# Performance work log

Hardware: AMD Instinct MI355X
Metric: run time of the kernel (lower is better)

Reference implementation:

```python
import jax, jax.numpy as jnp
import numpy as np

K = 3
STRIDE = 1
PAD = 1
EPS = 1e-5


def conv2d(x, w, b):
    # x [B,C,H,W], w [O,I,K,K], b [O]
    y = jax.lax.conv_general_dilated(
        x, w, (STRIDE, STRIDE), [(PAD, PAD), (PAD, PAD)],
        dimension_numbers=("NCHW", "OIHW", "NCHW"))
    return y + b[None, :, None, None]


def _bilinear_sample(img, py, px):
    # img [C,H,W]; py,px [KK,Ho,Wo] continuous coords; zero outside bounds
    H, W = img.shape[1], img.shape[2]
    y0 = jnp.floor(py)
    x0 = jnp.floor(px)
    wy1 = py - y0
    wx1 = px - x0
    wy0 = 1.0 - wy1
    wx0 = 1.0 - wx1

    def gather(yi, xi):
        valid = (yi >= 0) & (yi < H) & (xi >= 0) & (xi < W)
        yc = jnp.clip(yi, 0, H - 1).astype(jnp.int32)
        xc = jnp.clip(xi, 0, W - 1).astype(jnp.int32)
        v = img[:, yc, xc]  # [C,KK,Ho,Wo]
        return v * valid.astype(img.dtype)[None]

    out = (gather(y0, x0) * (wy0 * wx0)[None]
           + gather(y0, x0 + 1) * (wy0 * wx1)[None]
           + gather(y0 + 1, x0) * (wy1 * wx0)[None]
           + gather(y0 + 1, x0 + 1) * (wy1 * wx1)[None])
    return out  # [C,KK,Ho,Wo]


def deform_conv_bn_act(x, w_off, b_off, w_mod, b_mod, w_dc, gamma, beta):
    B, C, H, W = x.shape
    Cout = w_dc.shape[0]
    KK = K * K
    Ho = (H + 2 * PAD - K) // STRIDE + 1
    Wo = (W + 2 * PAD - K) // STRIDE + 1

    offset = conv2d(x, w_off, b_off)                 # [B,2*KK,Ho,Wo]
    modulation = jax.nn.sigmoid(conv2d(x, w_mod, b_mod))  # [B,KK,Ho,Wo]

    off = offset.reshape(B, KK, 2, Ho, Wo)
    dy, dx = off[:, :, 0], off[:, :, 1]              # [B,KK,Ho,Wo]

    ky = jnp.repeat(jnp.arange(K), K).astype(x.dtype)   # kernel row index per tap
    kx = jnp.tile(jnp.arange(K), K).astype(x.dtype)     # kernel col index per tap
    base_y = (jnp.arange(Ho, dtype=x.dtype) * STRIDE - PAD)[None, :, None] + ky[:, None, None]
    base_x = (jnp.arange(Wo, dtype=x.dtype) * STRIDE - PAD)[None, None, :] + kx[:, None, None]
    py = dy + base_y[None]                           # [B,KK,Ho,Wo]
    px = dx + base_x[None]

    sampled = jax.vmap(_bilinear_sample)(x, py, px)  # [B,C,KK,Ho,Wo]
    sampled = sampled * modulation[:, None]          # modulation per tap

    out = jnp.einsum("bckhw,ock->bohw", sampled, w_dc.reshape(Cout, C, KK))

    # BatchNorm (training-mode batch statistics, biased variance)
    mean = jnp.mean(out, axis=(0, 2, 3), keepdims=True)
    var = jnp.mean((out - mean) ** 2, axis=(0, 2, 3), keepdims=True)
    out = (out - mean) * jax.lax.rsqrt(var + EPS)
    out = out * gamma[None, :, None, None] + beta[None, :, None, None]

    return jax.nn.silu(out)


def setup_inputs() -> dict:
    key = jax.random.key(0)
    ks = jax.random.split(key, 8)
    B, Cin, Cout, H, W = 8, 128, 256, 64, 64
    x = jax.random.normal(ks[0], (B, Cin, H, W), dtype=jnp.float32)
    # small random offset/modulation weights (the literal init is all-zero, which
    # would make the deform conv degenerate to a plain conv)
    w_off = jax.random.normal(ks[1], (2 * K * K, Cin, K, K), dtype=jnp.float32) * 0.01
    b_off = jnp.zeros((2 * K * K,), dtype=jnp.float32)
    w_mod = jax.random.normal(ks[2], (K * K, Cin, K, K), dtype=jnp.float32) * 0.01
    b_mod = jnp.ones((K * K,), dtype=jnp.float32)
    fan_in = Cin * K * K
    w_dc = jax.random.normal(ks[3], (Cout, Cin, K, K), dtype=jnp.float32) / np.sqrt(fan_in)
    gamma = 1.0 + 0.1 * jax.random.normal(ks[4], (Cout,), dtype=jnp.float32)
    beta = 0.1 * jax.random.normal(ks[5], (Cout,), dtype=jnp.float32)
    return {"x": x, "w_off": w_off, "b_off": b_off, "w_mod": w_mod,
            "b_mod": b_mod, "w_dc": w_dc, "gamma": gamma, "beta": beta}


def reference(x, w_off, b_off, w_mod, b_mod, w_dc, gamma, beta):
    return deform_conv_bn_act(x, w_off, b_off, w_mod, b_mod, w_dc, gamma, beta)
```

## Files before the change

### kernel.cpp

```cpp
#include <hip/hip_runtime.h>
#include <hip/hip_bf16.h>
#include <math.h>

#define H_ 64
#define W_ 64
#define CIN 128
#define COUT 256
#define NB 8
#define KK9 9
#define NPIX 4096
#define KTOT 1152
#define NCK 36
#define KPAD 40

typedef short short8_t __attribute__((ext_vector_type(8)));
typedef float floatx4 __attribute__((ext_vector_type(4)));

__device__ __forceinline__ unsigned short f2bf(float f) {
    union { float f; unsigned u; } v; v.f = f;
    unsigned r = v.u + 0x7FFF + ((v.u >> 16) & 1);
    return (unsigned short)(r >> 16);
}
__device__ __forceinline__ float bf2f(unsigned short h) {
    union { unsigned u; float f; } v; v.u = ((unsigned)h) << 16;
    return v.f;
}

#if defined(__has_builtin)
#if __has_builtin(__builtin_amdgcn_global_load_lds)
#define HAVE_GLOAD_LDS 1
#endif
#endif

#ifdef HAVE_GLOAD_LDS
__device__ __forceinline__ void gload_lds16(const unsigned int* g, unsigned int* l) {
    __builtin_amdgcn_global_load_lds(
        (const __attribute__((address_space(1))) unsigned int*)g,
        (__attribute__((address_space(3))) unsigned int*)l, 16, 0, 0);
}
#endif

__global__ __launch_bounds__(256) void k_offmod(
    const float* __restrict__ x, const float* __restrict__ w_off,
    const float* __restrict__ b_off, const float* __restrict__ w_mod,
    const float* __restrict__ b_mod, float* __restrict__ ppy,
    float* __restrict__ ppx, float* __restrict__ pmod)
{
    __shared__ float xp[16][10][12];
    __shared__ float wb[27][16][12];
    const int t = threadIdx.x;
    const int tx = blockIdx.x, ty = blockIdx.y, b = blockIdx.z;
    const int q = t & 15, g = t >> 4;
    const int lpy = q >> 1, lpx4 = (q & 1) * 4;
    float acc[2][4] = {};

    for (int cc = 0; cc < CIN; cc += 16) {
        __syncthreads();
        for (int idx = t; idx < 1600; idx += 256) {
            int c = idx / 100, r = (idx % 100) / 10, col = idx % 10;
            int gy = ty * 8 - 1 + r, gx = tx * 8 - 1 + col;
            float v = 0.f;
            if (gy >= 0 && gy < H_ && gx >= 0 && gx < W_)
                v = x[((b * CIN + cc + c) * H_ + gy) * W_ + gx];
            xp[c][r][col] = v;
        }
        for (int idx = t; idx < 27 * 16 * 9; idx += 256) {
            int ch = idx / 144, rr = idx % 144, c = rr / 9, tap = rr % 9;
            wb[ch][c][tap] = (ch < 18)
                ? w_off[(ch * CIN + cc + c) * 9 + tap]
                : w_mod[((ch - 18) * CIN + cc + c) * 9 + tap];
        }
        __syncthreads();

        for (int c = 0; c < 16; ++c) {
            float xv[3][8];
            #pragma unroll
            for (int ky = 0; ky < 3; ++ky) {
                float4 v0 = *(const float4*)&xp[c][lpy + ky][lpx4];
                float4 v1 = *(const float4*)&xp[c][lpy + ky][lpx4 + 4];
                xv[ky][0] = v0.x; xv[ky][1] = v0.y; xv[ky][2] = v0.z; xv[ky][3] = v0.w;
                xv[ky][4] = v1.x; xv[ky][5] = v1.y; xv[ky][6] = v1.z; xv[ky][7] = v1.w;
            }
            #pragma unroll
            for (int i = 0; i < 2; ++i) {
                int ch = g + 16 * i;
                if (ch < 27) {
                    const float* wr = &wb[ch][c][0];
                    #pragma unroll
                    for (int ky = 0; ky < 3; ++ky)
                        #pragma unroll
                        for (int kx = 0; kx < 3; ++kx) {
                            float wv = wr[ky * 3 + kx];
                            #pragma unroll
                            for (int p = 0; p < 4; ++p)
                                acc[i][p] += xv[ky][p + kx] * wv;
                        }
                }
            }
        }
    }

    const int ho = ty * 8 + lpy;
    #pragma unroll
    for (int i = 0; i < 2; ++i) {
        int ch = g + 16 * i;
        if (ch >= 27) continue;
        #pragma unroll
        for (int p = 0; p < 4; ++p) {
            int wo = tx * 8 + lpx4 + p;
            int pix = ho * W_ + wo;
            if (ch < 18) {
                float v = acc[i][p] + b_off[ch];
                int kk = ch >> 1;
                if ((ch & 1) == 0)
                    ppy[(b * KK9 + kk) * NPIX + pix] = v + (float)(ho - 1 + kk / 3);
                else
                    ppx[(b * KK9 + kk) * NPIX + pix] = v + (float)(wo - 1 + kk % 3);
            } else {
                int km = ch - 18;
                float v = acc[i][p] + b_mod[km];
                pmod[(b * KK9 + km) * NPIX + pix] = 1.f / (1.f + expf(-v));
            }
        }
    }
}

__global__ __launch_bounds__(256) void k_prep(
    const float* __restrict__ w_dc, unsigned short* __restrict__ wsplit)
{
    int idx = blockIdx.x * 256 + threadIdx.x;
    int kl = idx % KPAD;
    int rest = idx / KPAD;
    int o = rest & 255;
    int rest2 = rest >> 8;
    int hl = rest2 & 1, ck = rest2 >> 1;
    unsigned short v = 0;
    if (kl < 32) {
        int kp = ck * 32 + kl;
        int kk = kp >> 7, c = kp & 127;
        float w = w_dc[o * KTOT + c * 9 + kk];
        unsigned short hi = f2bf(w);
        v = hl ? f2bf(w - bf2f(hi)) : hi;
    }
    wsplit[idx] = v;
}

__global__ __launch_bounds__(256, 2) void k_main(
    const float* __restrict__ x, const unsigned short* __restrict__ wsplit,
    const float* __restrict__ ppy, const float* __restrict__ ppx,
    const float* __restrict__ pmod, float* __restrict__ out,
    float* __restrict__ gsum, float* __restrict__ gsq)
{
    __shared__ __align__(16) unsigned short Wsp[2 * COUT * KPAD];
    __shared__ __align__(16) unsigned short Ssp[2 * 64 * KPAD];
    __shared__ float ppl[3][KK9][64];
    __shared__ float redS[COUT], redQ[COUT];

    const int t = threadIdx.x;
    const int b = blockIdx.x & 7;
    const int pix0 = (blockIdx.x >> 3) * 64;
    const int lane = t & 63, wm = t >> 6;

    for (int idx = t; idx < 3 * KK9 * 64; idx += 256) {
        int arr = idx / (KK9 * 64), rem = idx - arr * (KK9 * 64);
        int kk = rem >> 6, p = rem & 63;
        const float* src = (arr == 0) ? ppy : (arr == 1) ? ppx : pmod;
        ppl[arr][kk][p] = src[(b * KK9 + kk) * NPIX + pix0 + p];
    }
    __syncthreads();

    floatx4 acc[4][4] = {};
    const float* xb = x + b * CIN * NPIX;
    const int pxl = t & 63, kg = t >> 6;
    const int o_lane = lane & 15, g4 = lane >> 4;

    for (int kk = 0; kk < KK9; ++kk) {
        float py = ppl[0][kk][pxl];
        float px = ppl[1][kk][pxl];
        float m  = ppl[2][kk][pxl];
        float y0f = floorf(py), x0f = floorf(px);
        float wy1 = py - y0f, wx1 = px - x0f;
        float wy0 = 1.f - wy1, wx0 = 1.f - wx1;
        int y0 = (int)y0f, x0 = (int)x0f;
        bool y0v = (unsigned)y0 < (unsigned)H_;
        bool y1v = (unsigned)(y0 + 1) < (unsigned)H_;
        bool x0v = (unsigned)x0 < (unsigned)W_;
        bool x1v = (unsigned)(x0 + 1) < (unsigned)W_;
        float w00 = (y0v && x0v) ? wy0 * wx0 * m : 0.f;
        float w01 = (y0v && x1v) ? wy0 * wx1 * m : 0.f;
        float w10 = (y1v && x0v) ? wy1 * wx0 * m : 0.f;
        float w11 = (y1v && x1v) ? wy1 * wx1 * m : 0.f;
        int y0c = min(max(y0, 0), H_ - 1), y1c = min(max(y0 + 1, 0), H_ - 1);
        int x0c = min(max(x0, 0), W_ - 1), x1c = min(max(x0 + 1, 0), W_ - 1);
        int a00 = y0c * W_ + x0c, a01 = y0c * W_ + x1c;
        int a10 = y1c * W_ + x0c, a11 = y1c * W_ + x1c;

        for (int sub = 0; sub < 4; ++sub) {
            const int ck = kk * 4 + sub;
            __syncthreads();
            {
                const unsigned short* wsrc = wsplit + ck * (2 * COUT * KPAD);
#ifdef HAVE_GLOAD_LDS
                #pragma unroll
                for (int i = 0; i < 10; ++i) {
                    int slice = i * 4 + wm;
                    gload_lds16((const unsigned int*)(wsrc + slice * 512 + lane * 8),
                                (unsigned int*)(Wsp + slice * 512));
                }
#else
                const float4* s4 = (const float4*)wsrc;
                float4* d4 = (float4*)Wsp;
                #pragma unroll
                for (int i = 0; i < 10; ++i)
                    d4[i * 256 + t] = s4[i * 256 + t];
#endif
            }
            {
                const int c0 = sub * 32 + kg * 8;
                const float* pl = xb + c0 * NPIX;
                unsigned short hs[8], ls[8];
                #pragma unroll
                for (int j = 0; j < 8; ++j) {
                    float s = pl[a00] * w00 + pl[a01] * w01 +
                              pl[a10] * w10 + pl[a11] * w11;
                    union { float f; unsigned u; } su; su.f = s;
                    hs[j] = (unsigned short)(su.u >> 16);
                    union { unsigned u; float f; } hf; hf.u = su.u & 0xFFFF0000u;
                    union { float f; unsigned u; } du; du.f = s - hf.f;
                    ls[j] = (unsigned short)(du.u >> 16);
                    pl += NPIX;
                }
                union { unsigned short u[8]; short8_t v; } ph, plo;
                #pragma unroll
                for (int j = 0; j < 8; ++j) { ph.u[j] = hs[j]; plo.u[j] = ls[j]; }
                *(short8_t*)(Ssp + pxl * KPAD + kg * 8) = ph.v;
                *(short8_t*)(Ssp + 64 * KPAD + pxl * KPAD + kg * 8) = plo.v;
            }
            __syncthreads();

            short8_t bh[4], bl[4];
            #pragma unroll
            for (int ni = 0; ni < 4; ++ni) {
                int pxf = ni * 16 + o_lane;
                bh[ni] = *(const short8_t*)(Ssp + pxf * KPAD + g4 * 8);
                bl[ni] = *(const short8_t*)(Ssp + 64 * KPAD + pxf * KPAD + g4 * 8);
            }
            #pragma unroll
            for (int mi = 0; mi < 4; ++mi) {
                int of = wm * 64 + mi * 16 + o_lane;
                short8_t ah = *(const short8_t*)(Wsp + of * KPAD + g4 * 8);
                short8_t al = *(const short8_t*)(Wsp + COUT * KPAD + of * KPAD + g4 * 8);
                #pragma unroll
                for (int ni = 0; ni < 4; ++ni) {
                    acc[mi][ni] = __builtin_amdgcn_mfma_f32_16x16x32_bf16(
                        ah, bh[ni], acc[mi][ni], 0, 0, 0);
                    acc[mi][ni] = __builtin_amdgcn_mfma_f32_16x16x32_bf16(
                        ah, bl[ni], acc[mi][ni], 0, 0, 0);
                    acc[mi][ni] = __builtin_amdgcn_mfma_f32_16x16x32_bf16(
                        al, bh[ni], acc[mi][ni], 0, 0, 0);
                }
            }
        }
    }

    #pragma unroll
    for (int mi = 0; mi < 4; ++mi) {
        #pragma unroll
        for (int r = 0; r < 4; ++r) {
            float s = 0.f, q = 0.f;
            #pragma unroll
            for (int ni = 0; ni < 4; ++ni) {
                float v = acc[mi][ni][r];
                s += v; q += v * v;
            }
            s += __shfl_xor(s, 1); q += __shfl_xor(q, 1);
            s += __shfl_xor(s, 2); q += __shfl_xor(q, 2);
            s += __shfl_xor(s, 4); q += __shfl_xor(q, 4);
            s += __shfl_xor(s, 8); q += __shfl_xor(q, 8);
            if (o_lane == 0) {
                int o = wm * 64 + mi * 16 + g4 * 4 + r;
                redS[o] = s;
                redQ[o] = q;
            }
        }
    }
    __syncthreads();
    if (t < COUT) {
        atomicAdd(&gsum[t], redS[t]);
        atomicAdd(&gsq[t],  redQ[t]);
    }

    #pragma unroll
    for (int mi = 0; mi < 4; ++mi) {
        int o_base = wm * 64 + mi * 16 + g4 * 4;
        #pragma unroll
        for (int ni = 0; ni < 4; ++ni) {
            int px = pix0 + ni * 16 + o_lane;
            #pragma unroll
            for (int r = 0; r < 4; ++r)
                out[(b * COUT + o_base + r) * NPIX + px] = acc[mi][ni][r];
        }
    }
}

__global__ __launch_bounds__(256) void k_bnact(
    float* __restrict__ out, const float* __restrict__ gsum,
    const float* __restrict__ gsq, const float* __restrict__ gamma,
    const float* __restrict__ beta)
{
    int idx = blockIdx.x * 256 + threadIdx.x;
    int o = (idx >> 10) & 255;
    const float invn = 1.f / 32768.f;
    float mean = gsum[o] * invn;
    float var = gsq[o] * invn - mean * mean;
    float scale = gamma[o] * rsqrtf(var + 1e-5f);
    float shift = beta[o] - mean * scale;
    float4* p = (float4*)out;
    float4 v = p[idx];
    float y;
    y = v.x * scale + shift; v.x = y / (1.f + expf(-y));
    y = v.y * scale + shift; v.y = y / (1.f + expf(-y));
    y = v.z * scale + shift; v.z = y / (1.f + expf(-y));
    y = v.w * scale + shift; v.w = y / (1.f + expf(-y));
    p[idx] = v;
}

extern "C" void kernel_launch(void* const* d_in, const int* in_sizes, int n_in,
                              void* d_out, int out_size, void* d_ws, size_t ws_size,
                              hipStream_t stream)
{
    (void)in_sizes; (void)n_in; (void)out_size; (void)ws_size;
    const float* x     = (const float*)d_in[0];
    const float* w_off = (const float*)d_in[1];
    const float* b_off = (const float*)d_in[2];
    const float* w_mod = (const float*)d_in[3];
    const float* b_mod = (const float*)d_in[4];
    const float* w_dc  = (const float*)d_in[5];
    const float* gamma = (const float*)d_in[6];
    const float* beta  = (const float*)d_in[7];
    float* out = (float*)d_out;
    float* ws  = (float*)d_ws;

    const int NPK = NB * KK9 * NPIX;
    float* ppy  = ws;
    float* ppx  = ws + NPK;
    float* pmod = ws + 2 * NPK;
    unsigned short* wsplit = (unsigned short*)(ws + 3 * NPK);
    float* gsum = ws + 3 * NPK + 368640;
    float* gsq  = gsum + 256;

    hipMemsetAsync(gsum, 0, 512 * sizeof(float), stream);
    hipLaunchKernelGGL(k_offmod, dim3(8, 8, NB), dim3(256), 0, stream,
                       x, w_off, b_off, w_mod, b_mod, ppy, ppx, pmod);
    hipLaunchKernelGGL(k_prep, dim3(2880), dim3(256), 0, stream,
                       w_dc, wsplit);
    hipLaunchKernelGGL(k_main, dim3(512), dim3(256), 0, stream,
                       x, wsplit, ppy, ppx, pmod, out, gsum, gsq);
    hipLaunchKernelGGL(k_bnact, dim3(8192), dim3(256), 0, stream,
                       out, gsum, gsq, gamma, beta);
}
```

Baseline: 332.4 us.

## Double-buffer weight tiles, split output channels across blocks, software-pipeline gather

The main kernel now splits the 256 output channels into two halves per block, which doubles the grid to 1024 blocks and raises the occupancy hint to 3. Weight tiles are double-buffered in LDS through async global-to-LDS loads. The bilinear gather for the next K-chunk is issued before the MFMA phase of the current chunk, with explicit waitcnt and barriers. The weight layout in LDS switches from padding to an XOR swizzle, and the offset-conv kernel loads its filter taps as vectors. Together these aim to hide gather and weight-load latency behind MFMA work, at the cost of gathering the sampled input twice (once per channel half) and relying on hand-placed synchronisation.

```diff
diff --git a/kernel.cpp b/kernel.cpp
--- a/kernel.cpp
+++ b/kernel.cpp
@@ -11,7 +11,7 @@
 #define NPIX 4096
 #define KTOT 1152
 #define NCK 36
-#define KPAD 40
+#define SPAD 40
 
 typedef short short8_t __attribute__((ext_vector_type(8)));
 typedef float floatx4 __attribute__((ext_vector_type(4)));
@@ -33,12 +33,17 @@
 #endif
 
 #ifdef HAVE_GLOAD_LDS
-__device__ __forceinline__ void gload_lds16(const unsigned int* g, unsigned int* l) {
+__device__ __forceinline__ void gload_lds16(const unsigned short* g, unsigned short* l) {
     __builtin_amdgcn_global_load_lds(
         (const __attribute__((address_space(1))) unsigned int*)g,
         (__attribute__((address_space(3))) unsigned int*)l, 16, 0, 0);
 }
 #endif
+
+#define SBAR()   __builtin_amdgcn_s_barrier()
+#define SCHED0() __builtin_amdgcn_sched_barrier(0)
+#define WAIT_LGKM0() asm volatile("s_waitcnt lgkmcnt(0)" ::: "memory")
+#define WAIT_VM0()   asm volatile("s_waitcnt vmcnt(0)"   ::: "memory")
 
 __global__ __launch_bounds__(256) void k_offmod(
     const float* __restrict__ x, const float* __restrict__ w_off,
@@ -85,12 +90,16 @@
             for (int i = 0; i < 2; ++i) {
                 int ch = g + 16 * i;
                 if (ch < 27) {
-                    const float* wr = &wb[ch][c][0];
+                    float4 wa = *(const float4*)&wb[ch][c][0];
+                    float4 wv4 = *(const float4*)&wb[ch][c][4];
+                    float w8 = wb[ch][c][8];
+                    float wt[9] = {wa.x, wa.y, wa.z, wa.w,
+                                   wv4.x, wv4.y, wv4.z, wv4.w, w8};
                     #pragma unroll
                     for (int ky = 0; ky < 3; ++ky)
                         #pragma unroll
                         for (int kx = 0; kx < 3; ++kx) {
-                            float wv = wr[ky * 3 + kx];
+                            float wv = wt[ky * 3 + kx];
                             #pragma unroll
                             for (int p = 0; p < 4; ++p)
                                 acc[i][p] += xv[ky][p + kx] * wv;
@@ -129,55 +138,60 @@
     const float* __restrict__ w_dc, unsigned short* __restrict__ wsplit)
 {
     int idx = blockIdx.x * 256 + threadIdx.x;
-    int kl = idx % KPAD;
-    int rest = idx / KPAD;
-    int o = rest & 255;
-    int rest2 = rest >> 8;
-    int hl = rest2 & 1, ck = rest2 >> 1;
-    unsigned short v = 0;
-    if (kl < 32) {
-        int kp = ck * 32 + kl;
-        int kk = kp >> 7, c = kp & 127;
-        float w = w_dc[o * KTOT + c * 9 + kk];
-        unsigned short hi = f2bf(w);
-        v = hl ? f2bf(w - bf2f(hi)) : hi;
-    }
-    wsplit[idx] = v;
-}
-
-__global__ __launch_bounds__(256, 2) void k_main(
+    int klp = idx & 31;
+    int o = (idx >> 5) & 255;
+    int rest = idx >> 13;
+    int hl = rest & 1, ck = rest >> 1;
+    int g = (klp >> 3) ^ ((o >> 1) & 3);
+    int kl = g * 8 + (klp & 7);
+    int kp = ck * 32 + kl;
+    int kk = kp >> 7, c = kp & 127;
+    float w = w_dc[o * KTOT + c * 9 + kk];
+    unsigned short hi = f2bf(w);
+    wsplit[idx] = hl ? f2bf(w - bf2f(hi)) : hi;
+}
+
+__global__ __launch_bounds__(256, 3) void k_main(
     const float* __restrict__ x, const unsigned short* __restrict__ wsplit,
     const float* __restrict__ ppy, const float* __restrict__ ppx,
     const float* __restrict__ pmod, float* __restrict__ out,
     float* __restrict__ gsum, float* __restrict__ gsq)
 {
-    __shared__ __align__(16) unsigned short Wsp[2 * COUT * KPAD];
-    __shared__ __align__(16) unsigned short Ssp[2 * 64 * KPAD];
+    __shared__ __align__(16) unsigned short Wsp[2][2 * 128 * 32];
+    __shared__ __align__(16) unsigned short Ssp[2 * 64 * SPAD];
     __shared__ float ppl[3][KK9][64];
-    __shared__ float redS[COUT], redQ[COUT];
+    __shared__ float red[2][128][2];
 
     const int t = threadIdx.x;
     const int b = blockIdx.x & 7;
-    const int pix0 = (blockIdx.x >> 3) * 64;
-    const int lane = t & 63, wm = t >> 6;
+    const int rem = blockIdx.x >> 3;
+    const int oh = rem & 1;
+    const int pix0 = (rem >> 1) * 64;
+    const int lane = t & 63, wid = t >> 6;
+    const int wo = wid >> 1, wp = wid & 1;
+    const int o_lane = lane & 15, g4 = lane >> 4;
+    const int pxl = t & 63, kg = t >> 6;
 
     for (int idx = t; idx < 3 * KK9 * 64; idx += 256) {
-        int arr = idx / (KK9 * 64), rem = idx - arr * (KK9 * 64);
-        int kk = rem >> 6, p = rem & 63;
+        int arr = idx / (KK9 * 64), rem2 = idx - arr * (KK9 * 64);
+        int kk = rem2 >> 6, p = rem2 & 63;
         const float* src = (arr == 0) ? ppy : (arr == 1) ? ppx : pmod;
         ppl[arr][kk][p] = src[(b * KK9 + kk) * NPIX + pix0 + p];
     }
     __syncthreads();
 
-    floatx4 acc[4][4] = {};
+    floatx4 acc[4][2] = {};
     const float* xb = x + b * CIN * NPIX;
-    const int pxl = t & 63, kg = t >> 6;
-    const int o_lane = lane & 15, g4 = lane >> 4;
-
-    for (int kk = 0; kk < KK9; ++kk) {
-        float py = ppl[0][kk][pxl];
-        float px = ppl[1][kk][pxl];
-        float m  = ppl[2][kk][pxl];
+
+    float sreg[8];
+    float g00[8], g01[8], g10[8], g11[8];
+    float w00, w01, w10, w11;
+    int a00, a01, a10, a11;
+
+    auto SETUP = [&](int kkv) {
+        float py = ppl[0][kkv][pxl];
+        float px = ppl[1][kkv][pxl];
+        float m  = ppl[2][kkv][pxl];
         float y0f = floorf(py), x0f = floorf(px);
         float wy1 = py - y0f, wx1 = px - x0f;
         float wy0 = 1.f - wy1, wx0 = 1.f - wx1;
@@ -186,82 +200,109 @@
         bool y1v = (unsigned)(y0 + 1) < (unsigned)H_;
         bool x0v = (unsigned)x0 < (unsigned)W_;
         bool x1v = (unsigned)(x0 + 1) < (unsigned)W_;
-        float w00 = (y0v && x0v) ? wy0 * wx0 * m : 0.f;
-        float w01 = (y0v && x1v) ? wy0 * wx1 * m : 0.f;
-        float w10 = (y1v && x0v) ? wy1 * wx0 * m : 0.f;
-        float w11 = (y1v && x1v) ? wy1 * wx1 * m : 0.f;
+        w00 = (y0v && x0v) ? wy0 * wx0 * m : 0.f;
+        w01 = (y0v && x1v) ? wy0 * wx1 * m : 0.f;
+        w10 = (y1v && x0v) ? wy1 * wx0 * m : 0.f;
+        w11 = (y1v && x1v) ? wy1 * wx1 * m : 0.f;
         int y0c = min(max(y0, 0), H_ - 1), y1c = min(max(y0 + 1, 0), H_ - 1);
         int x0c = min(max(x0, 0), W_ - 1), x1c = min(max(x0 + 1, 0), W_ - 1);
-        int a00 = y0c * W_ + x0c, a01 = y0c * W_ + x1c;
-        int a10 = y1c * W_ + x0c, a11 = y1c * W_ + x1c;
-
-        for (int sub = 0; sub < 4; ++sub) {
-            const int ck = kk * 4 + sub;
-            __syncthreads();
-            {
-                const unsigned short* wsrc = wsplit + ck * (2 * COUT * KPAD);
+        a00 = y0c * W_ + x0c; a01 = y0c * W_ + x1c;
+        a10 = y1c * W_ + x0c; a11 = y1c * W_ + x1c;
+    };
+    auto GATHER = [&](int sub) {
+        const float* pl = xb + (sub * 32 + kg * 8) * NPIX;
+        #pragma unroll
+        for (int j = 0; j < 8; ++j) {
+            g00[j] = pl[a00]; g01[j] = pl[a01];
+            g10[j] = pl[a10]; g11[j] = pl[a11];
+            pl += NPIX;
+        }
+    };
+    auto CONSUME = [&]() {
+        #pragma unroll
+        for (int j = 0; j < 8; ++j)
+            sreg[j] = g00[j] * w00 + g01[j] * w01 + g10[j] * w10 + g11[j] * w11;
+    };
+    auto WRITES = [&]() {
+        union { unsigned short u[8]; short8_t v; } ph, plo;
+        #pragma unroll
+        for (int j = 0; j < 8; ++j) {
+            union { float f; unsigned u; } su; su.f = sreg[j];
+            ph.u[j] = (unsigned short)(su.u >> 16);
+            union { unsigned u; float f; } hf; hf.u = su.u & 0xFFFF0000u;
+            union { float f; unsigned u; } du; du.f = sreg[j] - hf.f;
+            plo.u[j] = (unsigned short)(du.u >> 16);
+        }
+        *(short8_t*)(Ssp + pxl * SPAD + kg * 8) = ph.v;
+        *(short8_t*)(Ssp + 64 * SPAD + pxl * SPAD + kg * 8) = plo.v;
+    };
+    auto GLOADW = [&](int ck, int buf) {
+        const unsigned short* wsrc = wsplit + ck * (2 * 256 * 32);
+        #pragma unroll
+        for (int i = 0; i < 4; ++i) {
+            int j2 = wid * 4 + i;
+            int hl = j2 >> 3, js = j2 & 7;
+            const unsigned short* src =
+                wsrc + (hl * 256 + oh * 128) * 32 + js * 512 + lane * 8;
+            unsigned short* dst = &Wsp[buf][hl * 4096 + js * 512];
 #ifdef HAVE_GLOAD_LDS
-                #pragma unroll
-                for (int i = 0; i < 10; ++i) {
-                    int slice = i * 4 + wm;
-                    gload_lds16((const unsigned int*)(wsrc + slice * 512 + lane * 8),
-                                (unsigned int*)(Wsp + slice * 512));
-                }
+            gload_lds16(src, dst);
 #else
-                const float4* s4 = (const float4*)wsrc;
-                float4* d4 = (float4*)Wsp;
-                #pragma unroll
-                for (int i = 0; i < 10; ++i)
-                    d4[i * 256 + t] = s4[i * 256 + t];
+            *(float4*)(dst + lane * 8) = *(const float4*)src;
 #endif
-            }
-            {
-                const int c0 = sub * 32 + kg * 8;
-                const float* pl = xb + c0 * NPIX;
-                unsigned short hs[8], ls[8];
-                #pragma unroll
-                for (int j = 0; j < 8; ++j) {
-                    float s = pl[a00] * w00 + pl[a01] * w01 +
-                              pl[a10] * w10 + pl[a11] * w11;
-                    union { float f; unsigned u; } su; su.f = s;
-                    hs[j] = (unsigned short)(su.u >> 16);
-                    union { unsigned u; float f; } hf; hf.u = su.u & 0xFFFF0000u;
-                    union { float f; unsigned u; } du; du.f = s - hf.f;
-                    ls[j] = (unsigned short)(du.u >> 16);
-                    pl += NPIX;
-                }
-                union { unsigned short u[8]; short8_t v; } ph, plo;
-                #pragma unroll
-                for (int j = 0; j < 8; ++j) { ph.u[j] = hs[j]; plo.u[j] = ls[j]; }
-                *(short8_t*)(Ssp + pxl * KPAD + kg * 8) = ph.v;
-                *(short8_t*)(Ssp + 64 * KPAD + pxl * KPAD + kg * 8) = plo.v;
-            }
-            __syncthreads();
-
-            short8_t bh[4], bl[4];
+        }
+    };
+    auto MFMA_PHASE = [&](int buf) {
+        short8_t bh[2], bl[2];
+        #pragma unroll
+        for (int ni = 0; ni < 2; ++ni) {
+            int pxf = wp * 32 + ni * 16 + o_lane;
+            bh[ni] = *(const short8_t*)(Ssp + pxf * SPAD + g4 * 8);
+            bl[ni] = *(const short8_t*)(Ssp + 64 * SPAD + pxf * SPAD + g4 * 8);
+        }
+        const int gsw = (g4 ^ ((o_lane >> 1) & 3)) << 3;
+        #pragma unroll
+        for (int mi = 0; mi < 4; ++mi) {
+            int row = wo * 64 + mi * 16 + o_lane;
+            const unsigned short* base = &Wsp[buf][row * 32 + gsw];
+            short8_t ah = *(const short8_t*)base;
+            short8_t al = *(const short8_t*)(base + 4096);
             #pragma unroll
-            for (int ni = 0; ni < 4; ++ni) {
-                int pxf = ni * 16 + o_lane;
-                bh[ni] = *(const short8_t*)(Ssp + pxf * KPAD + g4 * 8);
-                bl[ni] = *(const short8_t*)(Ssp + 64 * KPAD + pxf * KPAD + g4 * 8);
-            }
-            #pragma unroll
-            for (int mi = 0; mi < 4; ++mi) {
-                int of = wm * 64 + mi * 16 + o_lane;
-                short8_t ah = *(const short8_t*)(Wsp + of * KPAD + g4 * 8);
-                short8_t al = *(const short8_t*)(Wsp + COUT * KPAD + of * KPAD + g4 * 8);
-                #pragma unroll
-                for (int ni = 0; ni < 4; ++ni) {
-                    acc[mi][ni] = __builtin_amdgcn_mfma_f32_16x16x32_bf16(
-                        ah, bh[ni], acc[mi][ni], 0, 0, 0);
-                    acc[mi][ni] = __builtin_amdgcn_mfma_f32_16x16x32_bf16(
-                        ah, bl[ni], acc[mi][ni], 0, 0, 0);
-                    acc[mi][ni] = __builtin_amdgcn_mfma_f32_16x16x32_bf16(
-                        al, bh[ni], acc[mi][ni], 0, 0, 0);
-                }
-            }
-        }
-    }
+            for (int ni = 0; ni < 2; ++ni) {
+                acc[mi][ni] = __builtin_amdgcn_mfma_f32_16x16x32_bf16(
+                    ah, bh[ni], acc[mi][ni], 0, 0, 0);
+                acc[mi][ni] = __builtin_amdgcn_mfma_f32_16x16x32_bf16(
+                    ah, bl[ni], acc[mi][ni], 0, 0, 0);
+                acc[mi][ni] = __builtin_amdgcn_mfma_f32_16x16x32_bf16(
+                    al, bh[ni], acc[mi][ni], 0, 0, 0);
+            }
+        }
+    };
+
+    GLOADW(0, 0);
+    SCHED0();
+    SETUP(0);
+    GATHER(0);
+    CONSUME();
+
+    for (int tt = 0; tt < NCK - 1; ++tt) {
+        int buf = tt & 1;
+        WRITES();
+        GLOADW(tt + 1, buf ^ 1);
+        SCHED0();
+        SETUP((tt + 1) >> 2);
+        GATHER((tt + 1) & 3);
+        WAIT_LGKM0();
+        SBAR(); SCHED0();
+        MFMA_PHASE(buf);
+        CONSUME();
+        WAIT_VM0();
+        SCHED0(); SBAR(); SCHED0();
+    }
+    WRITES();
+    WAIT_LGKM0();
+    SBAR(); SCHED0();
+    MFMA_PHASE(1);
 
     #pragma unroll
     for (int mi = 0; mi < 4; ++mi) {
@@ -269,7 +310,7 @@
         for (int r = 0; r < 4; ++r) {
             float s = 0.f, q = 0.f;
             #pragma unroll
-            for (int ni = 0; ni < 4; ++ni) {
+            for (int ni = 0; ni < 2; ++ni) {
                 float v = acc[mi][ni][r];
                 s += v; q += v * v;
             }
@@ -278,24 +319,24 @@
             s += __shfl_xor(s, 4); q += __shfl_xor(q, 4);
             s += __shfl_xor(s, 8); q += __shfl_xor(q, 8);
             if (o_lane == 0) {
-                int o = wm * 64 + mi * 16 + g4 * 4 + r;
-                redS[o] = s;
-                redQ[o] = q;
+                int ol = wo * 64 + mi * 16 + g4 * 4 + r;
+                red[wp][ol][0] = s;
+                red[wp][ol][1] = q;
             }
         }
     }
     __syncthreads();
-    if (t < COUT) {
-        atomicAdd(&gsum[t], redS[t]);
-        atomicAdd(&gsq[t],  redQ[t]);
+    if (t < 128) {
+        atomicAdd(&gsum[oh * 128 + t], red[0][t][0] + red[1][t][0]);
+        atomicAdd(&gsq [oh * 128 + t], red[0][t][1] + red[1][t][1]);
     }
 
     #pragma unroll
     for (int mi = 0; mi < 4; ++mi) {
-        int o_base = wm * 64 + mi * 16 + g4 * 4;
-        #pragma unroll
-        for (int ni = 0; ni < 4; ++ni) {
-            int px = pix0 + ni * 16 + o_lane;
+        int o_base = oh * 128 + wo * 64 + mi * 16 + g4 * 4;
+        #pragma unroll
+        for (int ni = 0; ni < 2; ++ni) {
+            int px = pix0 + wp * 32 + ni * 16 + o_lane;
             #pragma unroll
             for (int r = 0; r < 4; ++r)
                 out[(b * COUT + o_base + r) * NPIX + px] = acc[mi][ni][r];
@@ -346,15 +387,15 @@
     float* ppx  = ws + NPK;
     float* pmod = ws + 2 * NPK;
     unsigned short* wsplit = (unsigned short*)(ws + 3 * NPK);
-    float* gsum = ws + 3 * NPK + 368640;
+    float* gsum = ws + 3 * NPK + 294912;
     float* gsq  = gsum + 256;
 
     hipMemsetAsync(gsum, 0, 512 * sizeof(float), stream);
     hipLaunchKernelGGL(k_offmod, dim3(8, 8, NB), dim3(256), 0, stream,
                        x, w_off, b_off, w_mod, b_mod, ppy, ppx, pmod);
-    hipLaunchKernelGGL(k_prep, dim3(2880), dim3(256), 0, stream,
+    hipLaunchKernelGGL(k_prep, dim3(2304), dim3(256), 0, stream,
                        w_dc, wsplit);
-    hipLaunchKernelGGL(k_main, dim3(512), dim3(256), 0, stream,
+    hipLaunchKernelGGL(k_main, dim3(1024), dim3(256), 0, stream,
                        x, wsplit, ppy, ppx, pmod, out, gsum, gsq);
     hipLaunchKernelGGL(k_bnact, dim3(8192), dim3(256), 0, stream,
                        out, gsum, gsq, gamma, beta);
```

Measured after the change: 395.2 us. +18.9%, slower.
